# Optimization experiments

Measured on AMD Instinct MI355X. Metric: run time of the kernel, lower is better.

Reference implementation:

```python
import jax, jax.numpy as jnp
import numpy as np

NEG_INF = -9e15  # matches the -9000000000000000.0 mask constant in the torch code
ALPHA = 0.2      # LeakyReLU negative slope


def setup_inputs() -> dict:
    key = jax.random.key(0)
    ks = jax.random.split(key, 8)
    N, F = 8192, 256
    h = jax.random.normal(ks[0], (N, F), dtype=jnp.float32)
    adj = jax.random.randint(ks[1], (N, N), 0, 2).astype(jnp.float32)
    W = jax.random.normal(ks[2], (F, F), dtype=jnp.float32) * 0.05
    a = jax.random.normal(ks[3], (2 * F, 1), dtype=jnp.float32) * 0.05
    w_ih = jax.random.normal(ks[4], (3 * F, F), dtype=jnp.float32) * 0.05
    w_hh = jax.random.normal(ks[5], (3 * F, F), dtype=jnp.float32) * 0.05
    b_ih = jax.random.normal(ks[6], (3 * F,), dtype=jnp.float32) * 0.05
    b_hh = jax.random.normal(ks[7], (3 * F,), dtype=jnp.float32) * 0.05
    return {"h": h, "adj": adj, "W": W, "a": a,
            "w_ih": w_ih, "w_hh": w_hh, "b_ih": b_ih, "b_hh": b_hh}


def reference(h, adj, W, a, w_ih, w_hh, b_ih, b_hh):
    F_out = W.shape[1]
    Wh = h @ W  # [N, F]
    # a_input @ a decomposes exactly: e_ij = leakyrelu(Wh_i . a[:F] + Wh_j . a[F:])
    src = Wh @ a[:F_out]   # [N, 1]
    dst = Wh @ a[F_out:]   # [N, 1]
    e = jax.nn.leaky_relu(src + dst.T, ALPHA)          # [N, N]
    att = jnp.where(adj > 0, e, NEG_INF)
    att = jax.nn.softmax(att, axis=1)                   # dropout: eval mode (identity)
    h_prime = att @ Wh                                  # [N, F]
    # torch GRUCell(h_prime, h)
    gi = h_prime @ w_ih.T + b_ih                        # [N, 3F]
    gh = h @ w_hh.T + b_hh
    i_r, i_z, i_n = jnp.split(gi, 3, axis=1)
    h_r, h_z, h_n = jnp.split(gh, 3, axis=1)
    r = jax.nn.sigmoid(i_r + h_r)
    z = jax.nn.sigmoid(i_z + h_z)
    n = jnp.tanh(i_n + r * h_n)
    return (1.0 - z) * n + z * h
```

## Files before the change

kernel.cpp:

```cpp
#include <hip/hip_runtime.h>

typedef __attribute__((ext_vector_type(8))) short bf16x8;
typedef __attribute__((ext_vector_type(4))) float f32x4;
typedef unsigned short u16;

#define NN 8192
#define FD 256

__device__ __forceinline__ u16 f2bf(float f) {
  union { float f; unsigned u; } v; v.f = f;
  unsigned r = v.u + 0x7FFF + ((v.u >> 16) & 1);
  return (u16)(r >> 16);
}

__device__ __forceinline__ bf16x8 ldcvt8(const float* __restrict__ p) {
  f32x4 x0 = *(const f32x4*)p;
  f32x4 x1 = *(const f32x4*)(p + 4);
  bf16x8 t;
  t[0] = (short)f2bf(x0[0]); t[1] = (short)f2bf(x0[1]);
  t[2] = (short)f2bf(x0[2]); t[3] = (short)f2bf(x0[3]);
  t[4] = (short)f2bf(x1[0]); t[5] = (short)f2bf(x1[1]);
  t[6] = (short)f2bf(x1[2]); t[7] = (short)f2bf(x1[3]);
  return t;
}

__global__ __launch_bounds__(256) void k_wh(const float* __restrict__ h,
                                            const float* __restrict__ W,
                                            const float* __restrict__ a,
                                            u16* __restrict__ whT,
                                            float* __restrict__ src,
                                            float* __restrict__ dst) {
  int tid = threadIdx.x;
  int lane = tid & 63;
  int wv = tid >> 6;
  int r0 = blockIdx.x * 64 + (wv >> 1) * 32;
  int c0 = blockIdx.y * 64 + (wv & 1) * 32;
  int lr = lane & 15;
  int q = lane >> 4;

  f32x4 acc[2][2] = {};
  for (int kk = 0; kk < FD; kk += 32) {
    int kb = kk + q * 8;
    bf16x8 av[2], bv[2];
#pragma unroll
    for (int m = 0; m < 2; m++)
      av[m] = ldcvt8(h + (size_t)(r0 + m * 16 + lr) * FD + kb);
#pragma unroll
    for (int n = 0; n < 2; n++) {
      int col = c0 + n * 16 + lr;
      const float* p = W + (size_t)kb * FD + col;
      bf16x8 t;
#pragma unroll
      for (int e = 0; e < 8; e++) t[e] = (short)f2bf(p[(size_t)e * FD]);
      bv[n] = t;
    }
#pragma unroll
    for (int m = 0; m < 2; m++)
#pragma unroll
      for (int n = 0; n < 2; n++)
        acc[m][n] = __builtin_amdgcn_mfma_f32_16x16x32_bf16(av[m], bv[n], acc[m][n], 0, 0, 0);
  }
#pragma unroll
  for (int m = 0; m < 2; m++)
#pragma unroll
    for (int n = 0; n < 2; n++) {
      int gc = c0 + n * 16 + lr;
      int gr = r0 + m * 16 + q * 4;
      ushort4 st;
      st.x = f2bf(acc[m][n][0]);
      st.y = f2bf(acc[m][n][1]);
      st.z = f2bf(acc[m][n][2]);
      st.w = f2bf(acc[m][n][3]);
      *(ushort4*)(whT + (size_t)gc * NN + gr) = st;
    }
  float aA0 = a[c0 + lr], aA1 = a[c0 + 16 + lr];
  float aB0 = a[256 + c0 + lr], aB1 = a[256 + c0 + 16 + lr];
#pragma unroll
  for (int m = 0; m < 2; m++)
#pragma unroll
    for (int j = 0; j < 4; j++) {
      float s1 = acc[m][0][j] * aA0 + acc[m][1][j] * aA1;
      float s2 = acc[m][0][j] * aB0 + acc[m][1][j] * aB1;
#pragma unroll
      for (int sh = 1; sh < 16; sh <<= 1) {
        s1 += __shfl_xor(s1, sh);
        s2 += __shfl_xor(s2, sh);
      }
      if (lr == 0) {
        int row = r0 + m * 16 + q * 4 + j;
        atomicAdd(&src[row], s1);
        atomicAdd(&dst[row], s2);
      }
    }
}

__global__ __launch_bounds__(512, 1) void k_att(const float* __restrict__ adj,
                                                const u16* __restrict__ whT,
                                                const float* __restrict__ src,
                                                const float* __restrict__ dst,
                                                float* __restrict__ hp,
                                                float* __restrict__ lg) {
  __shared__ u16 pbuf[3][8192];
  __shared__ float dst_lds[2048];
  __shared__ float lred[4][128];

  const int tid = threadIdx.x;
  const int lane = tid & 63;
  const int w = tid >> 6;
  const int lr = lane & 15;
  const int q = lane >> 4;
  const int bid = blockIdx.x;
  const int jh = bid & 3;
  const int i0 = (bid >> 2) * 128;
  const int jb = jh * 2048;

  const int pi = tid & 127;
  const int jg = tid >> 7;
  const float* adjP = adj + (size_t)(i0 + pi) * NN + jb + jg * 16;
  const float srcv = src[i0 + pi];
  const int c0 = w * 32;
  const u16* wp = whT + (size_t)(c0 + lr) * NN + jb + q * 8;
  const int pw0 = (pi * 64 + jg * 16) ^ ((pi & 7) << 3);
  const int pw1 = (pi * 64 + jg * 16 + 8) ^ ((pi & 7) << 3);

  f32x4 ar0[4], ar1[4];
  bf16x8 B0[2][2], B1[2][2];
  f32x4 acc[8][2] = {};
  float lsum = 0.f;

  *(f32x4*)&dst_lds[tid * 4] = *(const f32x4*)(dst + jb + tid * 4);

#define AL(S, AR)                                                              \
  { _Pragma("unroll") for (int v = 0; v < 4; v++)                              \
      AR[v] = *(const f32x4*)(adjP + (size_t)(S) * 64 + v * 4); }
#define BL(S, B)                                                               \
  { _Pragma("unroll") for (int kh = 0; kh < 2; kh++)                           \
    _Pragma("unroll") for (int n = 0; n < 2; n++)                              \
      B[kh][n] = *(const bf16x8*)(wp + (size_t)n * 16 * NN + (S) * 64 + kh * 32); }
#define PS(S, AR, WB)                                                          \
  {                                                                            \
    u16 pv[16];                                                                \
    _Pragma("unroll") for (int v = 0; v < 4; v++)                              \
      _Pragma("unroll") for (int e = 0; e < 4; e++) {                          \
        float x = srcv + dst_lds[(S) * 64 + jg * 16 + v * 4 + e];              \
        x = fmaxf(x, 0.2f * x);                                                \
        float p = AR[v][e] * __expf(x);                                        \
        lsum += p;                                                             \
        pv[v * 4 + e] = f2bf(p);                                               \
      }                                                                        \
    bf16x8 s0, s1;                                                             \
    _Pragma("unroll") for (int e = 0; e < 8; e++) {                            \
      s0[e] = (short)pv[e]; s1[e] = (short)pv[8 + e];                          \
    }                                                                          \
    *(bf16x8*)&pbuf[WB][pw0] = s0;                                             \
    *(bf16x8*)&pbuf[WB][pw1] = s1;                                             \
  }
#define CMPS(RB, B)                                                            \
  {                                                                            \
    _Pragma("unroll") for (int m = 0; m < 8; m++)                              \
      _Pragma("unroll") for (int kh = 0; kh < 2; kh++) {                       \
        bf16x8 pf = *(const bf16x8*)&pbuf[RB][((m * 16 + lr) * 64 + kh * 32 + q * 8) ^ ((lr & 7) << 3)]; \
        acc[m][0] = __builtin_amdgcn_mfma_f32_16x16x32_bf16(pf, B[kh][0], acc[m][0], 0, 0, 0); \
        acc[m][1] = __builtin_amdgcn_mfma_f32_16x16x32_bf16(pf, B[kh][1], acc[m][1], 0, 0, 0); \
      }                                                                        \
  }
#define LBAR asm volatile("s_waitcnt lgkmcnt(0)\n\ts_barrier" ::: "memory")

  AL(0, ar0);
  AL(1, ar1);
  BL(0, B0);
  __syncthreads();
  PS(0, ar0, 0);
  LBAR;

  int rb = 0, wb = 1;
  for (int t = 0; t < 32; t += 2) {
    if (t + 2 < 32) AL(t + 2, ar0);
    PS(t + 1, ar1, wb);
    BL(t + 1, B1);
    CMPS(rb, B0);
    LBAR;
    rb = wb; wb = (wb == 2) ? 0 : wb + 1;
    if (t + 3 < 32) AL(t + 3, ar1);
    if (t + 2 < 32) {
      PS(t + 2, ar0, wb);
      BL(t + 2, B0);
    }
    CMPS(rb, B1);
    LBAR;
    rb = wb; wb = (wb == 2) ? 0 : wb + 1;
  }
#undef AL
#undef BL
#undef PS
#undef CMPS
#undef LBAR

  lred[jg][pi] = lsum;
  __syncthreads();
  if (tid < 128) {
    float l = (lred[0][tid] + lred[1][tid]) + (lred[2][tid] + lred[3][tid]);
    atomicAdd(&lg[i0 + tid], l);
  }
#pragma unroll
  for (int m = 0; m < 8; m++)
#pragma unroll
    for (int n = 0; n < 2; n++)
#pragma unroll
      for (int j = 0; j < 4; j++)
        atomicAdd(&hp[(size_t)(i0 + m * 16 + q * 4 + j) * FD + c0 + n * 16 + lr],
                  acc[m][n][j]);
}

__global__ __launch_bounds__(256) void k_norm(const float* __restrict__ hp,
                                              const float* __restrict__ lg,
                                              u16* __restrict__ hpb) {
  int g = blockIdx.x * 1024 + threadIdx.x * 4;
  f32x4 v = *(const f32x4*)(hp + g);
  float inv = 1.0f / lg[g >> 8];
  ushort4 st;
  st.x = f2bf(v[0] * inv);
  st.y = f2bf(v[1] * inv);
  st.z = f2bf(v[2] * inv);
  st.w = f2bf(v[3] * inv);
  *(ushort4*)(hpb + g) = st;
}

__global__ __launch_bounds__(256) void k_gru(const u16* __restrict__ hpb,
                                             const float* __restrict__ h,
                                             const float* __restrict__ wih,
                                             const float* __restrict__ whh,
                                             const float* __restrict__ bih,
                                             const float* __restrict__ bhh,
                                             float* __restrict__ out) {
  int tid = threadIdx.x;
  int lane = tid & 63;
  int wv = tid >> 6;
  int i0 = blockIdx.x * 32;
  int lr = lane & 15;
  int q = lane >> 4;
  int c = blockIdx.y * 64 + wv * 16 + lr;
  f32x4 gi[3][2] = {};
  f32x4 gh[3][2] = {};
  for (int kk = 0; kk < FD; kk += 32) {
    int kb = kk + q * 8;
    bf16x8 ap[2], ah[2], bi[3], bh[3];
#pragma unroll
    for (int m = 0; m < 2; m++) {
      ap[m] = *(const bf16x8*)(hpb + (size_t)(i0 + m * 16 + lr) * FD + kb);
      ah[m] = ldcvt8(h + (size_t)(i0 + m * 16 + lr) * FD + kb);
    }
#pragma unroll
    for (int g = 0; g < 3; g++) {
      bi[g] = ldcvt8(wih + (size_t)(g * 256 + c) * FD + kb);
      bh[g] = ldcvt8(whh + (size_t)(g * 256 + c) * FD + kb);
    }
#pragma unroll
    for (int g = 0; g < 3; g++)
#pragma unroll
      for (int m = 0; m < 2; m++) {
        gi[g][m] = __builtin_amdgcn_mfma_f32_16x16x32_bf16(ap[m], bi[g], gi[g][m], 0, 0, 0);
        gh[g][m] = __builtin_amdgcn_mfma_f32_16x16x32_bf16(ah[m], bh[g], gh[g][m], 0, 0, 0);
      }
  }
  float bir = bih[c], biz = bih[256 + c], bin = bih[512 + c];
  float bhr = bhh[c], bhz = bhh[256 + c], bhn = bhh[512 + c];
#pragma unroll
  for (int m = 0; m < 2; m++)
#pragma unroll
    for (int j = 0; j < 4; j++) {
      int row = i0 + m * 16 + q * 4 + j;
      float rv = gi[0][m][j] + bir + gh[0][m][j] + bhr;
      float zv = gi[1][m][j] + biz + gh[1][m][j] + bhz;
      float r = 1.f / (1.f + __expf(-rv));
      float z = 1.f / (1.f + __expf(-zv));
      float nx = gi[2][m][j] + bin + r * (gh[2][m][j] + bhn);
      float n = 1.f - 2.f / (__expf(2.f * nx) + 1.f);
      float hv = h[(size_t)row * FD + c];
      out[(size_t)row * FD + c] = (1.f - z) * n + z * hv;
    }
}

extern "C" void kernel_launch(void* const* d_in, const int* in_sizes, int n_in,
                              void* d_out, int out_size, void* d_ws, size_t ws_size,
                              hipStream_t stream) {
  const float* h   = (const float*)d_in[0];
  const float* adj = (const float*)d_in[1];
  const float* W   = (const float*)d_in[2];
  const float* a   = (const float*)d_in[3];
  const float* wih = (const float*)d_in[4];
  const float* whh = (const float*)d_in[5];
  const float* bih = (const float*)d_in[6];
  const float* bhh = (const float*)d_in[7];
  float* out = (float*)d_out;

  char* ws = (char*)d_ws;
  u16* whT   = (u16*)(ws);
  u16* hpb   = (u16*)(ws);
  float* hp  = (float*)(ws + 4194304);
  float* lg  = (float*)(ws + 12582912);
  float* srcv = (float*)(ws + 12615680);
  float* dstv = (float*)(ws + 12648448);
  (void)ws_size;

  hipMemsetAsync(ws + 4194304, 0, 8486912, stream);
  k_wh<<<dim3(128, 4), 256, 0, stream>>>(h, W, a, whT, srcv, dstv);
  k_att<<<256, 512, 0, stream>>>(adj, whT, srcv, dstv, hp, lg);
  k_norm<<<2048, 256, 0, stream>>>(hp, lg, hpb);
  k_gru<<<dim3(256, 4), 256, 0, stream>>>(hpb, h, wih, whh, bih, bhh, out);
}
```

Before: 209.1 us.

## Halve attention row tile to raise occupancy and replace memset with zero kernel

The attention kernel now handles 64 rows per block instead of 128. That halves the LDS probability buffer and the accumulators, doubles the grid to 512 blocks, and raises launch bounds to allow several blocks per CU. Each wave now loads and converts 8 adjacency values per step rather than 16. The hipMemsetAsync is replaced with a custom vectorized zeroing kernel. The intent is better latency hiding and filling all CUs, at the cost of reloading the Wh tiles twice as often per row and doing more atomics on hp.

```diff
diff --git a/kernel.cpp b/kernel.cpp
--- a/kernel.cpp
+++ b/kernel.cpp
@@ -22,6 +22,12 @@
   t[4] = (short)f2bf(x1[0]); t[5] = (short)f2bf(x1[1]);
   t[6] = (short)f2bf(x1[2]); t[7] = (short)f2bf(x1[3]);
   return t;
+}
+
+__global__ __launch_bounds__(256) void k_zero(float* __restrict__ p) {
+  size_t g = (size_t)(blockIdx.x * 256 + threadIdx.x) * 4;
+  f32x4 z = {0.f, 0.f, 0.f, 0.f};
+  *(f32x4*)(p + g) = z;
 }
 
 __global__ __launch_bounds__(256) void k_wh(const float* __restrict__ h,
@@ -94,15 +100,15 @@
     }
 }
 
-__global__ __launch_bounds__(512, 1) void k_att(const float* __restrict__ adj,
+__global__ __launch_bounds__(512, 4) void k_att(const float* __restrict__ adj,
                                                 const u16* __restrict__ whT,
                                                 const float* __restrict__ src,
                                                 const float* __restrict__ dst,
                                                 float* __restrict__ hp,
                                                 float* __restrict__ lg) {
-  __shared__ u16 pbuf[3][8192];
+  __shared__ u16 pbuf[3][4096];
   __shared__ float dst_lds[2048];
-  __shared__ float lred[4][128];
+  __shared__ float lred[8][64];
 
   const int tid = threadIdx.x;
   const int lane = tid & 63;
@@ -111,53 +117,46 @@
   const int q = lane >> 4;
   const int bid = blockIdx.x;
   const int jh = bid & 3;
-  const int i0 = (bid >> 2) * 128;
+  const int i0 = (bid >> 2) * 64;
   const int jb = jh * 2048;
 
-  const int pi = tid & 127;
-  const int jg = tid >> 7;
-  const float* adjP = adj + (size_t)(i0 + pi) * NN + jb + jg * 16;
+  const int pi = lane;
+  const float* adjP = adj + (size_t)(i0 + pi) * NN + jb + w * 8;
   const float srcv = src[i0 + pi];
   const int c0 = w * 32;
   const u16* wp = whT + (size_t)(c0 + lr) * NN + jb + q * 8;
-  const int pw0 = (pi * 64 + jg * 16) ^ ((pi & 7) << 3);
-  const int pw1 = (pi * 64 + jg * 16 + 8) ^ ((pi & 7) << 3);
-
-  f32x4 ar0[4], ar1[4];
+  const int pw = (pi * 64 + w * 8) ^ ((pi & 7) << 3);
+
+  f32x4 ar0[2], ar1[2];
   bf16x8 B0[2][2], B1[2][2];
-  f32x4 acc[8][2] = {};
+  f32x4 acc[4][2] = {};
   float lsum = 0.f;
 
   *(f32x4*)&dst_lds[tid * 4] = *(const f32x4*)(dst + jb + tid * 4);
 
 #define AL(S, AR)                                                              \
-  { _Pragma("unroll") for (int v = 0; v < 4; v++)                              \
-      AR[v] = *(const f32x4*)(adjP + (size_t)(S) * 64 + v * 4); }
+  { AR[0] = *(const f32x4*)(adjP + (size_t)(S) * 64);                          \
+    AR[1] = *(const f32x4*)(adjP + (size_t)(S) * 64 + 4); }
 #define BL(S, B)                                                               \
   { _Pragma("unroll") for (int kh = 0; kh < 2; kh++)                           \
     _Pragma("unroll") for (int n = 0; n < 2; n++)                              \
       B[kh][n] = *(const bf16x8*)(wp + (size_t)n * 16 * NN + (S) * 64 + kh * 32); }
 #define PS(S, AR, WB)                                                          \
   {                                                                            \
-    u16 pv[16];                                                                \
-    _Pragma("unroll") for (int v = 0; v < 4; v++)                              \
+    bf16x8 s0;                                                                 \
+    _Pragma("unroll") for (int v = 0; v < 2; v++)                              \
       _Pragma("unroll") for (int e = 0; e < 4; e++) {                          \
-        float x = srcv + dst_lds[(S) * 64 + jg * 16 + v * 4 + e];              \
+        float x = srcv + dst_lds[(S) * 64 + w * 8 + v * 4 + e];                \
         x = fmaxf(x, 0.2f * x);                                                \
         float p = AR[v][e] * __expf(x);                                        \
         lsum += p;                                                             \
-        pv[v * 4 + e] = f2bf(p);                                               \
+        s0[v * 4 + e] = (short)f2bf(p);                                        \
       }                                                                        \
-    bf16x8 s0, s1;                                                             \
-    _Pragma("unroll") for (int e = 0; e < 8; e++) {                            \
-      s0[e] = (short)pv[e]; s1[e] = (short)pv[8 + e];                          \
-    }                                                                          \
-    *(bf16x8*)&pbuf[WB][pw0] = s0;                                             \
-    *(bf16x8*)&pbuf[WB][pw1] = s1;                                             \
+    *(bf16x8*)&pbuf[WB][pw] = s0;                                              \
   }
 #define CMPS(RB, B)                                                            \
   {                                                                            \
-    _Pragma("unroll") for (int m = 0; m < 8; m++)                              \
+    _Pragma("unroll") for (int m = 0; m < 4; m++)                              \
       _Pragma("unroll") for (int kh = 0; kh < 2; kh++) {                       \
         bf16x8 pf = *(const bf16x8*)&pbuf[RB][((m * 16 + lr) * 64 + kh * 32 + q * 8) ^ ((lr & 7) << 3)]; \
         acc[m][0] = __builtin_amdgcn_mfma_f32_16x16x32_bf16(pf, B[kh][0], acc[m][0], 0, 0, 0); \
@@ -196,14 +195,16 @@
 #undef CMPS
 #undef LBAR
 
-  lred[jg][pi] = lsum;
+  lred[w][pi] = lsum;
   __syncthreads();
-  if (tid < 128) {
-    float l = (lred[0][tid] + lred[1][tid]) + (lred[2][tid] + lred[3][tid]);
+  if (tid < 64) {
+    float l = 0.f;
+#pragma unroll
+    for (int v = 0; v < 8; v++) l += lred[v][tid];
     atomicAdd(&lg[i0 + tid], l);
   }
 #pragma unroll
-  for (int m = 0; m < 8; m++)
+  for (int m = 0; m < 4; m++)
 #pragma unroll
     for (int n = 0; n < 2; n++)
 #pragma unroll
@@ -303,9 +304,9 @@
   float* dstv = (float*)(ws + 12648448);
   (void)ws_size;
 
-  hipMemsetAsync(ws + 4194304, 0, 8486912, stream);
+  k_zero<<<2072, 256, 0, stream>>>((float*)(ws + 4194304));
   k_wh<<<dim3(128, 4), 256, 0, stream>>>(h, W, a, whT, srcv, dstv);
-  k_att<<<256, 512, 0, stream>>>(adj, whT, srcv, dstv, hp, lg);
+  k_att<<<512, 512, 0, stream>>>(adj, whT, srcv, dstv, hp, lg);
   k_norm<<<2048, 256, 0, stream>>>(hp, lg, hpb);
   k_gru<<<dim3(256, 4), 256, 0, stream>>>(hpb, h, wih, whh, bih, bhh, out);
 }
```

New measurement: 215.9 us. +3.3%, slower.
